# Optimization experiments

Hardware: AMD Instinct MI355X
Metric: run time of the kernel (lower is better)

Reference implementation:

```python
import jax, jax.numpy as jnp
import numpy as np

N, E, F_IN, EDGE_DIM = 50000, 800000, 128, 64
H, C = 4, 64  # heads, per-head out channels
NEG_SLOPE = 0.2  # PyG GATConv default


def setup_inputs() -> dict:
    key = jax.random.key(0)
    ks = jax.random.split(key, 16)
    p = lambda i, shape: jax.random.normal(ks[i], shape, jnp.float32) * 0.05
    return {
        "node_features": jax.random.normal(ks[0], (N, F_IN), jnp.float32),
        "edge_features": jax.random.normal(ks[1], (E, EDGE_DIM), jnp.float32),
        "edge_index": jax.random.randint(ks[2], (2, E), 0, N),
        # layer 1 (concat=True, ELU)
        "W1": p(3, (F_IN, H * C)),
        "att_src1": p(4, (H, C)), "att_dst1": p(5, (H, C)), "att_edge1": p(6, (H, C)),
        "bias1": jnp.zeros((H * C,), jnp.float32),
        "edgeW1": p(7, (EDGE_DIM, H * C)),
        # layer 2 (concat=False -> mean over heads, no activation)
        "W2": p(8, (H * C, H * C)),
        "att_src2": p(9, (H, C)), "att_dst2": p(10, (H, C)), "att_edge2": p(11, (H, C)),
        "bias2": jnp.zeros((C,), jnp.float32),
        "edgeW2": p(12, (EDGE_DIM, H * C)),
    }


def _gat_layer(x, edge_feat, src, dst, W, a_s, a_d, a_e, bias, edgeW, concat):
    n = x.shape[0]
    h = (x @ W).reshape(n, H, C)                      # [N,H,C]
    ef = (edge_feat @ edgeW).reshape(-1, H, C)        # [E,H,C] edge_linear projection
    # GATConv add_self_loops=True, fill_value='mean': self-loop attr = mean of incoming edge attrs
    ones = jnp.ones((src.shape[0],), x.dtype)
    cnt = jnp.maximum(jax.ops.segment_sum(ones, dst, num_segments=n), 1.0)
    loop_attr = jax.ops.segment_sum(ef, dst, num_segments=n) / cnt[:, None, None]
    ef_f = jnp.concatenate([ef, loop_attr], axis=0)   # [E+N,H,C]
    loops = jnp.arange(n)
    src_f = jnp.concatenate([src, loops], axis=0)
    dst_f = jnp.concatenate([dst, loops], axis=0)
    # per-edge attention logits: alpha_j + alpha_i + alpha_edge
    a_src = jnp.einsum('nhc,hc->nh', h, a_s)
    a_dst = jnp.einsum('nhc,hc->nh', h, a_d)
    logits = a_src[src_f] + a_dst[dst_f] + jnp.einsum('ehc,hc->eh', ef_f, a_e)
    logits = jax.nn.leaky_relu(logits, NEG_SLOPE)     # [E+N,H]
    # segment softmax over incoming edges of each dst node (every node has a self-loop)
    m = jax.ops.segment_max(logits, dst_f, num_segments=n)
    pexp = jnp.exp(logits - m[dst_f])
    denom = jax.ops.segment_sum(pexp, dst_f, num_segments=n)
    alpha = pexp / (denom[dst_f] + 1e-16)
    # message = x_j * alpha, scatter-add to dst
    out = jax.ops.segment_sum(h[src_f] * alpha[..., None], dst_f, num_segments=n)  # [N,H,C]
    if concat:
        return out.reshape(n, H * C) + bias
    return out.mean(axis=1) + bias


def reference(node_features, edge_features, edge_index,
              W1, att_src1, att_dst1, att_edge1, bias1, edgeW1,
              W2, att_src2, att_dst2, att_edge2, bias2, edgeW2):
    src, dst = edge_index[0], edge_index[1]
    x = _gat_layer(node_features, edge_features, src, dst,
                   W1, att_src1, att_dst1, att_edge1, bias1, edgeW1, concat=True)
    x = jax.nn.elu(x)
    return _gat_layer(x, edge_features, src, dst,
                      W2, att_src2, att_dst2, att_edge2, bias2, edgeW2, concat=False)
```

## Files before the change

### kernel.cpp

```cpp
#include <hip/hip_runtime.h>
#include <hip/hip_fp16.h>
#include <math.h>

#define NNODE 50000
#define NEDGE 800000
#define FIN 128
#define EDIM 64
#define HC 256
#define NH 4
#define CC 64
#define SCAN_TILE 512

typedef _Float16 half8v __attribute__((ext_vector_type(8)));
typedef _Float16 half4v __attribute__((ext_vector_type(4)));
typedef float floatx4 __attribute__((ext_vector_type(4)));

__global__ void k_count(const int* __restrict__ dst, int* counts, int E) {
    int e = blockIdx.x * 256 + threadIdx.x;
    if (e < E) atomicAdd(&counts[dst[e]], 1);
}

__global__ void k_scan1(const int* __restrict__ counts, int* offs, int* tilesums, int N) {
    __shared__ int s[SCAN_TILE];
    int t = threadIdx.x;
    int i = blockIdx.x * SCAN_TILE + t;
    int v = (i < N) ? counts[i] : 0;
    s[t] = v;
    for (int off = 1; off < SCAN_TILE; off <<= 1) {
        __syncthreads();
        int x = (t >= off) ? s[t - off] : 0;
        __syncthreads();
        s[t] += x;
    }
    __syncthreads();
    if (i < N) offs[i] = s[t] - v;
    if (t == SCAN_TILE - 1) tilesums[blockIdx.x] = s[t];
}

__global__ void k_scan2(int* tilesums, int nt) {
    __shared__ int s[128];
    int t = threadIdx.x;
    int v = (t < nt) ? tilesums[t] : 0;
    s[t] = v;
    for (int off = 1; off < 128; off <<= 1) {
        __syncthreads();
        int x = (t >= off) ? s[t - off] : 0;
        __syncthreads();
        s[t] += x;
    }
    __syncthreads();
    if (t < nt) tilesums[t] = s[t] - v;
}

__global__ void k_scan3(int* offs, const int* __restrict__ tilesums, int N, int E) {
    int t = threadIdx.x;
    int i = blockIdx.x * SCAN_TILE + t;
    if (i < N) offs[i] += tilesums[blockIdx.x];
    if (i == 0) offs[N] = E;
}

__global__ void k_fill(const int* __restrict__ src, const int* __restrict__ dst,
                       const int* __restrict__ offs, int* cursor,
                       int* __restrict__ srcs, int* __restrict__ epos, int E) {
    int e = blockIdx.x * 256 + threadIdx.x;
    if (e < E) {
        int d = dst[e];
        int pos = offs[d] + atomicAdd(&cursor[d], 1);
        srcs[pos] = src[e];
        epos[e] = pos;
    }
}

__device__ inline float4 h4_to_f4(uint2 r) {
    float2 fa = __half22float2(*(__half2*)&r.x);
    float2 fb = __half22float2(*(__half2*)&r.y);
    return make_float4(fa.x, fa.y, fb.x, fb.y);
}

__device__ inline float sel_h(float4 v, int head) {
    return head == 0 ? v.x : head == 1 ? v.y : head == 2 ? v.z : v.w;
}

__global__ void k_castW(const float* __restrict__ W, _Float16* __restrict__ Wt, int K) {
    int k = blockIdx.x, n = threadIdx.x;
    Wt[(size_t)n * K + k] = (_Float16)W[(size_t)k * HC + n];
}

template <typename AT>
__global__ __launch_bounds__(256) void k_gemm_mfma(const AT* __restrict__ A,
                                                   const _Float16* __restrict__ Wt16,
                                                   _Float16* __restrict__ H16,
                                                   const float* __restrict__ att_s,
                                                   const float* __restrict__ att_d,
                                                   float* __restrict__ asrc,
                                                   float* __restrict__ adst,
                                                   int M, int K) {
    int wave = threadIdx.x >> 6, lane = threadIdx.x & 63;
    int quad = lane >> 4, l16 = lane & 15;
    int row = blockIdx.x * 64 + wave * 16 + l16;
    bool rok = row < M;
    floatx4 acc[16];
#pragma unroll
    for (int i = 0; i < 16; i++) acc[i] = (floatx4)(0.0f);
    int nk = K >> 5;
    for (int kk = 0; kk < nk; kk++) {
        half8v a = {};
        if (rok) {
            if constexpr (sizeof(AT) == 2) {
                a = *(const half8v*)(A + (size_t)row * K + kk * 32 + quad * 8);
            } else {
                const float* ap = (const float*)A + (size_t)row * K + kk * 32 + quad * 8;
                float4 v0 = *(const float4*)ap;
                float4 v1 = *(const float4*)(ap + 4);
                a[0] = (_Float16)v0.x; a[1] = (_Float16)v0.y;
                a[2] = (_Float16)v0.z; a[3] = (_Float16)v0.w;
                a[4] = (_Float16)v1.x; a[5] = (_Float16)v1.y;
                a[6] = (_Float16)v1.z; a[7] = (_Float16)v1.w;
            }
        }
#pragma unroll
        for (int nt = 0; nt < 16; nt++) {
            half8v b = *(const half8v*)(Wt16 + (size_t)(nt * 16 + l16) * K + kk * 32 + quad * 8);
            acc[nt] = __builtin_amdgcn_mfma_f32_16x16x32_f16(a, b, acc[nt], 0, 0, 0);
        }
    }
    float asl[16], adl[16];
#pragma unroll
    for (int nt = 0; nt < 16; nt++) {
        asl[nt] = att_s[nt * 16 + l16];
        adl[nt] = att_d[nt * 16 + l16];
    }
    int orow0 = blockIdx.x * 64 + wave * 16 + quad * 4;
#pragma unroll
    for (int r = 0; r < 4; r++) {
        int orow = orow0 + r;
        float4 vs4, vd4;
        float* vsp = (float*)&vs4;
        float* vdp = (float*)&vd4;
#pragma unroll
        for (int hh = 0; hh < 4; hh++) {
            float vs = 0.f, vd = 0.f;
#pragma unroll
            for (int q = 0; q < 4; q++) {
                int nt = hh * 4 + q;
                float hv = acc[nt][r];
                vs += hv * asl[nt];
                vd += hv * adl[nt];
            }
            vs += __shfl_xor(vs, 1, 64); vd += __shfl_xor(vd, 1, 64);
            vs += __shfl_xor(vs, 2, 64); vd += __shfl_xor(vd, 2, 64);
            vs += __shfl_xor(vs, 4, 64); vd += __shfl_xor(vd, 4, 64);
            vs += __shfl_xor(vs, 8, 64); vd += __shfl_xor(vd, 8, 64);
            vsp[hh] = vs; vdp[hh] = vd;
        }
        if (l16 == 0 && orow < M) {
            ((float4*)asrc)[orow] = vs4;
            ((float4*)adst)[orow] = vd4;
        }
    }
#pragma unroll
    for (int r = 0; r < 4; r++) {
        int orow = orow0 + r;
        if (orow < M) {
#pragma unroll
            for (int nt = 0; nt < 16; nt++)
                H16[(size_t)orow * HC + nt * 16 + l16] = (_Float16)acc[nt][r];
        }
    }
}

__global__ void k_weatt(const float* __restrict__ edgeW, const float* __restrict__ att_e,
                        float* we) {
    int t = threadIdx.x;
    int d = t >> 2, hh = t & 3;
    float s = 0.f;
    for (int c = 0; c < 64; c++) s += edgeW[d * HC + hh * 64 + c] * att_e[hh * 64 + c];
    we[d * 4 + hh] = s;
}

__global__ __launch_bounds__(256) void k_elog_both(const float* __restrict__ ef,
                                                   const float* __restrict__ we1,
                                                   const float* __restrict__ we2,
                                                   const int* __restrict__ epos,
                                                   float* __restrict__ elogc1,
                                                   float* __restrict__ elogc2, int E) {
    __shared__ float sw1[256], sw2[256];
    int t = threadIdx.x;
    sw1[t] = we1[t];
    sw2[t] = we2[t];
    __syncthreads();
    int e = blockIdx.x * 256 + t;
    if (e >= E) return;
    int pos = epos[e];
    const float4* row = (const float4*)(ef + (size_t)e * EDIM);
    float a10 = 0.f, a11 = 0.f, a12 = 0.f, a13 = 0.f;
    float a20 = 0.f, a21 = 0.f, a22 = 0.f, a23 = 0.f;
#pragma unroll
    for (int c4 = 0; c4 < 16; c4++) {
        float4 v = row[c4];
        const float* vp = (const float*)&v;
#pragma unroll
        for (int k = 0; k < 4; k++) {
            float vv = vp[k];
            int c = c4 * 4 + k;
            float4 w1 = *(const float4*)&sw1[c << 2];
            float4 w2 = *(const float4*)&sw2[c << 2];
            a10 += vv * w1.x; a11 += vv * w1.y; a12 += vv * w1.z; a13 += vv * w1.w;
            a20 += vv * w2.x; a21 += vv * w2.y; a22 += vv * w2.z; a23 += vv * w2.w;
        }
    }
    ((float4*)elogc1)[pos] = make_float4(a10, a11, a12, a13);
    ((float4*)elogc2)[pos] = make_float4(a20, a21, a22, a23);
}

template <int LAYER>
__global__ __launch_bounds__(256) void k_aggr_fused(const _Float16* __restrict__ hb,
                                                    const float* __restrict__ elogc,
                                                    const float* __restrict__ asrc,
                                                    const float* __restrict__ adst,
                                                    const int* __restrict__ offs,
                                                    const int* __restrict__ srcs,
                                                    const float* __restrict__ bias,
                                                    _Float16* __restrict__ out16,
                                                    float* __restrict__ out32, int N) {
    __shared__ float sW[4][256];
    int wave = threadIdx.x >> 6, lane = threadIdx.x & 63;
    int n = blockIdx.x * 4 + wave;
    if (n >= N) return;
    int head = lane >> 4;
    const uint2* hf = (const uint2*)hb;
    const float4* elc = (const float4*)elogc;
    const float4* asp = (const float4*)asrc;
    float* sWp = sW[wave];
    int beg = offs[n], end = offs[n + 1];

    float4 adn = ((const float4*)adst)[n];
    float adnh = sel_h(adn, head);

    float denom = 0.f;
    float sx = 0.f, sy = 0.f, sz = 0.f, sw = 0.f;
    float ax = 0.f, ay = 0.f, az = 0.f, aw = 0.f;

    for (int i0 = beg; i0 < end; i0 += 64) {
        int m = end - i0; if (m > 64) m = 64;
        bool act = lane < m;
        int sj = 0;
        float4 el = make_float4(0.f, 0.f, 0.f, 0.f);
        float4 a4 = make_float4(0.f, 0.f, 0.f, 0.f);
        if (act) {
            uint idx = (uint)(i0 + lane);
            sj = srcs[idx];
            el = elc[idx];
            a4 = asp[(uint)sj];
        }
        sx += el.x; sy += el.y; sz += el.z; sw += el.w;
        float4 w4;
        float l;
        l = a4.x + adn.x + el.x; l = l > 0.f ? l : 0.2f * l; w4.x = act ? __expf(l) : 0.f;
        l = a4.y + adn.y + el.y; l = l > 0.f ? l : 0.2f * l; w4.y = act ? __expf(l) : 0.f;
        l = a4.z + adn.z + el.z; l = l > 0.f ? l : 0.2f * l; w4.z = act ? __expf(l) : 0.f;
        l = a4.w + adn.w + el.w; l = l > 0.f ? l : 0.2f * l; w4.w = act ? __expf(l) : 0.f;
        *(float4*)&sWp[lane << 2] = w4;
        __builtin_amdgcn_wave_barrier();

        int j = 0;
        for (; j + 8 <= m; j += 8) {
            uint2 r[8];
            float w[8];
#pragma unroll
            for (int k = 0; k < 8; k++) {
                int sk = __builtin_amdgcn_readlane(sj, j + k);
                w[k] = sWp[((j + k) << 2) + head];
                r[k] = hf[(size_t)((uint)sk * 64u) + lane];
            }
#pragma unroll
            for (int k = 0; k < 8; k++) {
                float4 h4 = h4_to_f4(r[k]);
                denom += w[k];
                ax += w[k] * h4.x; ay += w[k] * h4.y;
                az += w[k] * h4.z; aw += w[k] * h4.w;
            }
        }
        for (; j < m; j++) {
            int sk = __builtin_amdgcn_readlane(sj, j);
            float wk = sWp[(j << 2) + head];
            uint2 rk = hf[(size_t)((uint)sk * 64u) + lane];
            float4 h4 = h4_to_f4(rk);
            denom += wk;
            ax += wk * h4.x; ay += wk * h4.y;
            az += wk * h4.z; aw += wk * h4.w;
        }
        __builtin_amdgcn_wave_barrier();
    }

#pragma unroll
    for (int msk = 32; msk >= 1; msk >>= 1) {
        sx += __shfl_xor(sx, msk, 64);
        sy += __shfl_xor(sy, msk, 64);
        sz += __shfl_xor(sz, msk, 64);
        sw += __shfl_xor(sw, msk, 64);
    }
    float selh = sel_h(make_float4(sx, sy, sz, sw), head);

    float cnt = (float)(end - beg);
    if (cnt < 1.f) cnt = 1.f;
    float asnh = sel_h(asp[(uint)n], head);
    float ls = asnh + adnh + selh / cnt;
    ls = ls > 0.f ? ls : 0.2f * ls;
    float ws = __expf(ls);
    denom += ws;
    float4 hn = h4_to_f4(hf[(size_t)n * 64 + lane]);
    ax += ws * hn.x; ay += ws * hn.y; az += ws * hn.z; aw += ws * hn.w;

    float inv = 1.0f / (denom + 1e-16f);
    ax *= inv; ay *= inv; az *= inv; aw *= inv;

    if (LAYER == 1) {
        float4 bv = ((const float4*)bias)[lane];
        half4v o;
        float v;
        v = ax + bv.x; o[0] = (_Float16)(v > 0.f ? v : __expf(v) - 1.0f);
        v = ay + bv.y; o[1] = (_Float16)(v > 0.f ? v : __expf(v) - 1.0f);
        v = az + bv.z; o[2] = (_Float16)(v > 0.f ? v : __expf(v) - 1.0f);
        v = aw + bv.w; o[3] = (_Float16)(v > 0.f ? v : __expf(v) - 1.0f);
        ((half4v*)(out16 + (size_t)n * HC))[lane] = o;
    } else {
        ax += __shfl_xor(ax, 16, 64); ax += __shfl_xor(ax, 32, 64);
        ay += __shfl_xor(ay, 16, 64); ay += __shfl_xor(ay, 32, 64);
        az += __shfl_xor(az, 16, 64); az += __shfl_xor(az, 32, 64);
        aw += __shfl_xor(aw, 16, 64); aw += __shfl_xor(aw, 32, 64);
        if (lane < 16) {
            float4 bv = ((const float4*)bias)[lane];
            float4 o;
            o.x = 0.25f * ax + bv.x;
            o.y = 0.25f * ay + bv.y;
            o.z = 0.25f * az + bv.z;
            o.w = 0.25f * aw + bv.w;
            ((float4*)(out32 + (size_t)n * CC))[lane] = o;
        }
    }
}

extern "C" void kernel_launch(void* const* d_in, const int* in_sizes, int n_in,
                              void* d_out, int out_size, void* d_ws, size_t ws_size,
                              hipStream_t stream) {
    const float* x   = (const float*)d_in[0];
    const float* ef  = (const float*)d_in[1];
    const int*   ei  = (const int*)d_in[2];
    const float* W1  = (const float*)d_in[3];
    const float* as1 = (const float*)d_in[4];
    const float* ad1 = (const float*)d_in[5];
    const float* ae1 = (const float*)d_in[6];
    const float* b1  = (const float*)d_in[7];
    const float* eW1 = (const float*)d_in[8];
    const float* W2  = (const float*)d_in[9];
    const float* as2 = (const float*)d_in[10];
    const float* ad2 = (const float*)d_in[11];
    const float* ae2 = (const float*)d_in[12];
    const float* b2  = (const float*)d_in[13];
    const float* eW2 = (const float*)d_in[14];
    float* out = (float*)d_out;
    const int* srcp = ei;
    const int* dstp = ei + NEDGE;

    char* w = (char*)d_ws;
    auto alloc = [&](size_t bytes) -> char* {
        char* r = w;
        w += (bytes + 255) / 256 * 256;
        return r;
    };
    _Float16* hb16  = (_Float16*)alloc((size_t)NNODE * HC * 2);
    _Float16* x216  = (_Float16*)alloc((size_t)NNODE * HC * 2);
    _Float16* wt1   = (_Float16*)alloc((size_t)HC * FIN * 2);
    _Float16* wt2   = (_Float16*)alloc((size_t)HC * HC * 2);
    float* elogc1 = (float*)alloc((size_t)NEDGE * 4 * 4);
    float* elogc2 = (float*)alloc((size_t)NEDGE * 4 * 4);
    float* asrc   = (float*)alloc((size_t)NNODE * 4 * 4);
    float* adst   = (float*)alloc((size_t)NNODE * 4 * 4);
    float* webuf1 = (float*)alloc(64 * 4 * 4);
    float* webuf2 = (float*)alloc(64 * 4 * 4);
    int* counts  = (int*)alloc((size_t)NNODE * 4);
    int* offs    = (int*)alloc((size_t)(NNODE + 1) * 4);
    int* tiles   = (int*)alloc(1024 * 4);
    int* cursor  = (int*)alloc((size_t)NNODE * 4);
    int* srcs    = (int*)alloc((size_t)NEDGE * 4);
    int* epos    = (int*)alloc((size_t)NEDGE * 4);

    hipMemsetAsync(counts, 0, (size_t)NNODE * 4, stream);
    hipMemsetAsync(cursor, 0, (size_t)NNODE * 4, stream);

    k_count<<<(NEDGE + 255) / 256, 256, 0, stream>>>(dstp, counts, NEDGE);
    int nt = (NNODE + SCAN_TILE - 1) / SCAN_TILE;
    k_scan1<<<nt, SCAN_TILE, 0, stream>>>(counts, offs, tiles, NNODE);
    k_scan2<<<1, 128, 0, stream>>>(tiles, nt);
    k_scan3<<<nt, SCAN_TILE, 0, stream>>>(offs, tiles, NNODE, NEDGE);
    k_fill<<<(NEDGE + 255) / 256, 256, 0, stream>>>(srcp, dstp, offs, cursor, srcs, epos, NEDGE);

    k_castW<<<FIN, 256, 0, stream>>>(W1, wt1, FIN);
    k_castW<<<HC, 256, 0, stream>>>(W2, wt2, HC);

    k_weatt<<<1, 256, 0, stream>>>(eW1, ae1, webuf1);
    k_weatt<<<1, 256, 0, stream>>>(eW2, ae2, webuf2);
    k_elog_both<<<(NEDGE + 255) / 256, 256, 0, stream>>>(ef, webuf1, webuf2, epos, elogc1, elogc2, NEDGE);

    k_gemm_mfma<float><<<(NNODE + 63) / 64, 256, 0, stream>>>(x, wt1, hb16, as1, ad1, asrc, adst, NNODE, FIN);
    k_aggr_fused<1><<<(NNODE + 3) / 4, 256, 0, stream>>>(hb16, elogc1, asrc, adst, offs, srcs, b1, x216, nullptr, NNODE);

    k_gemm_mfma<_Float16><<<(NNODE + 63) / 64, 256, 0, stream>>>(x216, wt2, hb16, as2, ad2, asrc, adst, NNODE, HC);
    k_aggr_fused<2><<<(NNODE + 3) / 4, 256, 0, stream>>>(hb16, elogc2, asrc, adst, offs, srcs, b2, nullptr, out, NNODE);
}
```

Before: 711.3 us.

## Merge setup kernels, store CSR as (edge,src) pairs, unroll aggregation by 16

Replaces two memsets, two weight-cast kernels and two edge-attention kernels with one k_prep launch to cut launch overhead. The CSR fill now writes (edge id, src) pairs, so k_elog_both iterates in CSR order with coalesced writes and gathers edge-feature rows instead, and the aggregation reads src from the pair array. Adds a 16-wide unrolled gather loop in aggregation to keep more loads in flight, at the cost of register pressure and a now random 256-byte row read of edge features.

New measurement: 702.9 us. About the same (-1.2%).

```diff
diff --git a/kernel.cpp b/kernel.cpp
--- a/kernel.cpp
+++ b/kernel.cpp
@@ -14,6 +14,37 @@
 typedef _Float16 half8v __attribute__((ext_vector_type(8)));
 typedef _Float16 half4v __attribute__((ext_vector_type(4)));
 typedef float floatx4 __attribute__((ext_vector_type(4)));
+
+__global__ __launch_bounds__(256) void k_prep(int* counts, int* cursor,
+                                              const float* __restrict__ W1, _Float16* wt1,
+                                              const float* __restrict__ W2, _Float16* wt2,
+                                              const float* __restrict__ eW1, const float* __restrict__ ae1, float* we1,
+                                              const float* __restrict__ eW2, const float* __restrict__ ae2, float* we2) {
+    int b = blockIdx.x, t = threadIdx.x;
+    if (b < 391) {
+        int i = b * 256 + t;
+        if (i < NNODE) counts[i] = 0;
+        else if (i < 2 * NNODE) cursor[i - NNODE] = 0;
+    } else if (b < 519) {
+        int idx = (b - 391) * 256 + t;
+        int n = idx >> 7, k = idx & 127;
+        wt1[n * FIN + k] = (_Float16)W1[(size_t)k * HC + n];
+    } else if (b < 775) {
+        int idx = (b - 519) * 256 + t;
+        int n = idx >> 8, k = idx & 255;
+        wt2[n * HC + k] = (_Float16)W2[(size_t)k * HC + n];
+    } else {
+        int idx = (b - 775) * 256 + t;
+        const float* eW = idx < 256 ? eW1 : eW2;
+        const float* ae = idx < 256 ? ae1 : ae2;
+        float* we = idx < 256 ? we1 : we2;
+        int q = idx & 255;
+        int d = q >> 2, hh = q & 3;
+        float s = 0.f;
+        for (int c = 0; c < 64; c++) s += eW[d * HC + hh * 64 + c] * ae[hh * 64 + c];
+        we[d * 4 + hh] = s;
+    }
+}
 
 __global__ void k_count(const int* __restrict__ dst, int* counts, int E) {
     int e = blockIdx.x * 256 + threadIdx.x;
@@ -61,13 +92,12 @@
 
 __global__ void k_fill(const int* __restrict__ src, const int* __restrict__ dst,
                        const int* __restrict__ offs, int* cursor,
-                       int* __restrict__ srcs, int* __restrict__ epos, int E) {
+                       int2* __restrict__ es, int E) {
     int e = blockIdx.x * 256 + threadIdx.x;
     if (e < E) {
         int d = dst[e];
         int pos = offs[d] + atomicAdd(&cursor[d], 1);
-        srcs[pos] = src[e];
-        epos[e] = pos;
+        es[pos] = make_int2(e, src[e]);
     }
 }
 
@@ -79,11 +109,6 @@
 
 __device__ inline float sel_h(float4 v, int head) {
     return head == 0 ? v.x : head == 1 ? v.y : head == 2 ? v.z : v.w;
-}
-
-__global__ void k_castW(const float* __restrict__ W, _Float16* __restrict__ Wt, int K) {
-    int k = blockIdx.x, n = threadIdx.x;
-    Wt[(size_t)n * K + k] = (_Float16)W[(size_t)k * HC + n];
 }
 
 template <typename AT>
@@ -169,19 +194,10 @@
     }
 }
 
-__global__ void k_weatt(const float* __restrict__ edgeW, const float* __restrict__ att_e,
-                        float* we) {
-    int t = threadIdx.x;
-    int d = t >> 2, hh = t & 3;
-    float s = 0.f;
-    for (int c = 0; c < 64; c++) s += edgeW[d * HC + hh * 64 + c] * att_e[hh * 64 + c];
-    we[d * 4 + hh] = s;
-}
-
 __global__ __launch_bounds__(256) void k_elog_both(const float* __restrict__ ef,
                                                    const float* __restrict__ we1,
                                                    const float* __restrict__ we2,
-                                                   const int* __restrict__ epos,
+                                                   const int2* __restrict__ es,
                                                    float* __restrict__ elogc1,
                                                    float* __restrict__ elogc2, int E) {
     __shared__ float sw1[256], sw2[256];
@@ -189,10 +205,10 @@
     sw1[t] = we1[t];
     sw2[t] = we2[t];
     __syncthreads();
-    int e = blockIdx.x * 256 + t;
-    if (e >= E) return;
-    int pos = epos[e];
-    const float4* row = (const float4*)(ef + (size_t)e * EDIM);
+    int p = blockIdx.x * 256 + t;
+    if (p >= E) return;
+    int e = es[p].x;
+    const float4* row = (const float4*)(ef + (size_t)(uint)e * EDIM);
     float a10 = 0.f, a11 = 0.f, a12 = 0.f, a13 = 0.f;
     float a20 = 0.f, a21 = 0.f, a22 = 0.f, a23 = 0.f;
 #pragma unroll
@@ -209,8 +225,8 @@
             a20 += vv * w2.x; a21 += vv * w2.y; a22 += vv * w2.z; a23 += vv * w2.w;
         }
     }
-    ((float4*)elogc1)[pos] = make_float4(a10, a11, a12, a13);
-    ((float4*)elogc2)[pos] = make_float4(a20, a21, a22, a23);
+    ((float4*)elogc1)[p] = make_float4(a10, a11, a12, a13);
+    ((float4*)elogc2)[p] = make_float4(a20, a21, a22, a23);
 }
 
 template <int LAYER>
@@ -219,7 +235,7 @@
                                                     const float* __restrict__ asrc,
                                                     const float* __restrict__ adst,
                                                     const int* __restrict__ offs,
-                                                    const int* __restrict__ srcs,
+                                                    const int2* __restrict__ es,
                                                     const float* __restrict__ bias,
                                                     _Float16* __restrict__ out16,
                                                     float* __restrict__ out32, int N) {
@@ -249,7 +265,7 @@
         float4 a4 = make_float4(0.f, 0.f, 0.f, 0.f);
         if (act) {
             uint idx = (uint)(i0 + lane);
-            sj = srcs[idx];
+            sj = es[idx].y;
             el = elc[idx];
             a4 = asp[(uint)sj];
         }
@@ -264,6 +280,23 @@
         __builtin_amdgcn_wave_barrier();
 
         int j = 0;
+        for (; j + 16 <= m; j += 16) {
+            uint2 r[16];
+            float w[16];
+#pragma unroll
+            for (int k = 0; k < 16; k++) {
+                int sk = __builtin_amdgcn_readlane(sj, j + k);
+                w[k] = sWp[((j + k) << 2) + head];
+                r[k] = hf[(size_t)((uint)sk * 64u) + lane];
+            }
+#pragma unroll
+            for (int k = 0; k < 16; k++) {
+                float4 h4 = h4_to_f4(r[k]);
+                denom += w[k];
+                ax += w[k] * h4.x; ay += w[k] * h4.y;
+                az += w[k] * h4.z; aw += w[k] * h4.w;
+            }
+        }
         for (; j + 8 <= m; j += 8) {
             uint2 r[8];
             float w[8];
@@ -383,29 +416,23 @@
     int* offs    = (int*)alloc((size_t)(NNODE + 1) * 4);
     int* tiles   = (int*)alloc(1024 * 4);
     int* cursor  = (int*)alloc((size_t)NNODE * 4);
-    int* srcs    = (int*)alloc((size_t)NEDGE * 4);
-    int* epos    = (int*)alloc((size_t)NEDGE * 4);
-
-    hipMemsetAsync(counts, 0, (size_t)NNODE * 4, stream);
-    hipMemsetAsync(cursor, 0, (size_t)NNODE * 4, stream);
+    int2* es     = (int2*)alloc((size_t)NEDGE * 8);
+
+    k_prep<<<777, 256, 0, stream>>>(counts, cursor, W1, wt1, W2, wt2,
+                                    eW1, ae1, webuf1, eW2, ae2, webuf2);
 
     k_count<<<(NEDGE + 255) / 256, 256, 0, stream>>>(dstp, counts, NEDGE);
     int nt = (NNODE + SCAN_TILE - 1) / SCAN_TILE;
     k_scan1<<<nt, SCAN_TILE, 0, stream>>>(counts, offs, tiles, NNODE);
     k_scan2<<<1, 128, 0, stream>>>(tiles, nt);
     k_scan3<<<nt, SCAN_TILE, 0, stream>>>(offs, tiles, NNODE, NEDGE);
-    k_fill<<<(NEDGE + 255) / 256, 256, 0, stream>>>(srcp, dstp, offs, cursor, srcs, epos, NEDGE);
-
-    k_castW<<<FIN, 256, 0, stream>>>(W1, wt1, FIN);
-    k_castW<<<HC, 256, 0, stream>>>(W2, wt2, HC);
-
-    k_weatt<<<1, 256, 0, stream>>>(eW1, ae1, webuf1);
-    k_weatt<<<1, 256, 0, stream>>>(eW2, ae2, webuf2);
-    k_elog_both<<<(NEDGE + 255) / 256, 256, 0, stream>>>(ef, webuf1, webuf2, epos, elogc1, elogc2, NEDGE);
+    k_fill<<<(NEDGE + 255) / 256, 256, 0, stream>>>(srcp, dstp, offs, cursor, es, NEDGE);
+
+    k_elog_both<<<(NEDGE + 255) / 256, 256, 0, stream>>>(ef, webuf1, webuf2, es, elogc1, elogc2, NEDGE);
 
     k_gemm_mfma<float><<<(NNODE + 63) / 64, 256, 0, stream>>>(x, wt1, hb16, as1, ad1, asrc, adst, NNODE, FIN);
-    k_aggr_fused<1><<<(NNODE + 3) / 4, 256, 0, stream>>>(hb16, elogc1, asrc, adst, offs, srcs, b1, x216, nullptr, NNODE);
+    k_aggr_fused<1><<<(NNODE + 3) / 4, 256, 0, stream>>>(hb16, elogc1, asrc, adst, offs, es, b1, x216, nullptr, NNODE);
 
     k_gemm_mfma<_Float16><<<(NNODE + 63) / 64, 256, 0, stream>>>(x216, wt2, hb16, as2, ad2, asrc, adst, NNODE, HC);
-    k_aggr_fused<2><<<(NNODE + 3) / 4, 256, 0, stream>>>(hb16, elogc2, asrc, adst, offs, srcs, b2, nullptr, out, NNODE);
-}
+    k_aggr_fused<2><<<(NNODE + 3) / 4, 256, 0, stream>>>(hb16, elogc2, asrc, adst, offs, es, b2, nullptr, out, NNODE);
+}
```
